# Performance work log

Hardware: AMD Instinct MI355X
Metric: run time of the kernel (lower is better)

Reference implementation:

```python
import jax, jax.numpy as jnp
from jax import lax
import numpy as np

B, T, L, D, TOPK, KC = 8, 4096, 256, 128, 8, 9  # KC = ctx conv kernel size


def setup_inputs() -> dict:
    key = jax.random.key(0)
    ks = jax.random.split(key, 9)
    s = 0.05
    return {
        "x": jax.random.normal(ks[0], (B, T), jnp.float32),
        "lag_embed": jax.random.normal(ks[1], (L + 1, D), jnp.float32) * s,  # nn.Embedding(L+1, d)
        "val_w": jax.random.normal(ks[2], (D, 1), jnp.float32) * s,          # nn.Linear(1, d) weight
        "val_b": jnp.zeros((D,), jnp.float32),
        "conv_w": jax.random.normal(ks[3], (D, 1, KC), jnp.float32) * s,     # Conv1d(1, d, 9) weight (O,I,K)
        "conv_b": jnp.zeros((D,), jnp.float32),
        "ctx_w": jax.random.normal(ks[4], (D, D), jnp.float32) * s,          # ctx_proj
        "ctx_b": jnp.zeros((D,), jnp.float32),
        "wq": jax.random.normal(ks[5], (D, D), jnp.float32) * s,             # Wq (no bias)
        "wk": jax.random.normal(ks[6], (D, D), jnp.float32) * s,             # Wk (no bias)
        "bias_w": jax.random.normal(ks[7], (1, D), jnp.float32) * s,         # bias_head
        "bias_b": jnp.zeros((1,), jnp.float32),
    }


def _lag_bank(x, Lv):
    # Xlags[b, t, l] = x[b, t-(l+1)], left-padded with zeros (per docstring/intended math)
    Bv, Tv = x.shape
    pads = jnp.pad(x, ((0, 0), (Lv, 0)))
    idx = Lv - 1 + jnp.arange(Tv)[:, None] - jnp.arange(Lv)[None, :]  # (T, L)
    return pads[:, idx]  # (B, T, L)


def reference(x, lag_embed, val_w, val_b, conv_w, conv_b, ctx_w, ctx_b, wq, wk, bias_w, bias_b):
    Xlags = _lag_bank(x, L)  # (B, T, L)

    # Causal context conv: left-pad 8 zeros, Conv1d(1, D, 9, padding=0)
    xp = jnp.pad(x, ((0, 0), (KC - 1, 0)))[:, None, :]  # (B, 1, T+8)
    ctx = lax.conv_general_dilated(xp, conv_w, (1,), 'VALID',
                                   dimension_numbers=('NCH', 'OIH', 'NCH'))
    ctx = ctx + conv_b[None, :, None]           # (B, D, T)
    ctx = jnp.transpose(ctx, (0, 2, 1))         # (B, T, D)
    ctx = ctx @ ctx_w.T + ctx_b                 # ctx_proj

    q = ctx @ wq.T                              # (B, T, D)
    # score = <q, Wk Hlag> = <Wk^T q, Hlag>; Hlag = Xlags*val_w + (val_b + lag_embed[1:L+1])
    # is rank-1 in the value -> never materialize the (B,T,L,D) tensor.
    qk = q @ wk                                 # (B, T, D) = Wk^T q
    base = val_b[None, :] + lag_embed[1:L + 1]  # (L, D)
    logits = Xlags * (qk @ val_w[:, 0])[:, :, None] + qk @ base.T  # (B, T, L)

    # top-k sparsification (ties are measure-zero with continuous inputs)
    kth = lax.top_k(logits, TOPK)[0][..., -1:]
    masked = jnp.where(logits >= kth, logits, -jnp.inf)
    w = jax.nn.softmax(masked, axis=-1)         # (B, T, L)

    mu = jnp.sum(w * Xlags, axis=-1) + (ctx @ bias_w.T)[..., 0] + bias_b[0]  # (B, T)
    return mu, w
```

## Files before the change

kernel.cpp:

```cpp
#include <hip/hip_runtime.h>
#include <math.h>

#define D   128
#define LQ  256
#define KCQ 9
#define BQ  8
#define TQ  4096
#define RISK_DELTA 2e-5f
#define WCAP 16384

__global__ void pk1(const float* __restrict__ wk, const float* __restrict__ wq,
                    const float* __restrict__ ctx_w, const float* __restrict__ bias_w,
                    const float* __restrict__ conv_w, const float* __restrict__ val_b,
                    const float* __restrict__ lag_embed,
                    double* __restrict__ T2, double* __restrict__ u, int* __restrict__ wcnt,
                    float* __restrict__ ctx_wT, float* __restrict__ wqT,
                    float* __restrict__ conv_wT, float* __restrict__ baseT) {
    int tid = threadIdx.x;
    int bid = blockIdx.x;
    if (bid < D) {
        int d = bid;
        if (tid < D) {
            double acc = 0.0;
            for (int j = 0; j < D; ++j)
                acc += (double)wk[j * D + d] * (double)wq[j * D + tid];
            T2[d * D + tid] = acc;
            ctx_wT[d * D + tid] = ctx_w[tid * D + d];
            wqT[d * D + tid]    = wq[tid * D + d];
            if (d < KCQ) conv_wT[d * D + tid] = conv_w[tid * KCQ + d];
        }
        baseT[d * LQ + tid] = __fadd_rn(val_b[d], lag_embed[(size_t)(tid + 1) * D + d]);
    } else if (bid == D) {
        if (tid < D) {
            double acc = 0.0;
            for (int dd = 0; dd < D; ++dd)
                acc += (double)bias_w[dd] * (double)ctx_w[dd * D + tid];
            u[tid] = acc;
        }
    } else {
        if (tid == 0) *wcnt = 0;
    }
}

__global__ void pk2(const double* __restrict__ T2, const float* __restrict__ ctx_w,
                    const float* __restrict__ conv_w, const float* __restrict__ conv_b,
                    const float* __restrict__ ctx_b,
                    double* __restrict__ g, double* __restrict__ c1) {
    __shared__ double row[D];
    int d = blockIdx.x, e = threadIdx.x;
    double acc = 0.0;
    for (int j = 0; j < D; ++j)
        acc += T2[d * D + j] * (double)ctx_w[j * D + e];
    row[e] = acc;
    __syncthreads();
    if (e < KCQ) {
        double a = 0.0;
        for (int q = 0; q < D; ++q) a += row[q] * (double)conv_w[q * KCQ + e];
        g[e * D + d] = a;
    } else if (e == KCQ) {
        double a = 0.0;
        for (int q = 0; q < D; ++q) a += row[q] * (double)conv_b[q];
        for (int q = 0; q < D; ++q) a += T2[d * D + q] * (double)ctx_b[q];
        c1[d] = a;
    }
}

__global__ void pk3(const float* __restrict__ lag_embed, const float* __restrict__ val_b,
                    const float* __restrict__ val_w, const float* __restrict__ conv_w,
                    const float* __restrict__ conv_b, const float* __restrict__ ctx_b,
                    const float* __restrict__ bias_w, const float* __restrict__ bias_b,
                    const double* __restrict__ g, const double* __restrict__ c1,
                    const double* __restrict__ u,
                    double* __restrict__ gbT, double* __restrict__ cbv, double* __restrict__ cst) {
    int tid = threadIdx.x;
    if (blockIdx.x < LQ) {
        __shared__ double bl[D];
        int l = blockIdx.x;
        bl[tid] = (double)val_b[tid] + (double)lag_embed[(l + 1) * D + tid];
        __syncthreads();
        if (tid < KCQ) {
            double a = 0.0;
            for (int q = 0; q < D; ++q) a += bl[q] * g[tid * D + q];
            gbT[tid * LQ + l] = a;
        } else if (tid == KCQ) {
            double a = 0.0;
            for (int q = 0; q < D; ++q) a += bl[q] * c1[q];
            cbv[l] = a;
        }
    } else {
        if (tid < KCQ) {
            double a = 0.0, a2 = 0.0;
            for (int q = 0; q < D; ++q) a  += g[tid * D + q] * (double)val_w[q];
            for (int q = 0; q < D; ++q) a2 += u[q] * (double)conv_w[q * KCQ + tid];
            cst[tid]      = a;
            cst[10 + tid] = a2;
        } else if (tid == KCQ) {
            double a = 0.0, a2 = 0.0;
            for (int q = 0; q < D; ++q) a  += c1[q] * (double)val_w[q];
            for (int q = 0; q < D; ++q) a2 += u[q] * (double)conv_b[q];
            for (int q = 0; q < D; ++q) a2 += (double)bias_w[q] * (double)ctx_b[q];
            cst[9]  = a;
            cst[19] = a2 + (double)bias_b[0];
        }
    }
}

__global__ __launch_bounds__(256, 4) void lag_main(
    const float* __restrict__ x, const double* __restrict__ gbT,
    const double* __restrict__ cbv, const double* __restrict__ cst,
    float* __restrict__ muOut, float* __restrict__ wOut,
    int* __restrict__ wcnt, int* __restrict__ wlist) {
    __shared__ float sgb[KCQ * LQ];
    __shared__ float scb[LQ];
    __shared__ float sc[20];
    int tid = threadIdx.x;
    #pragma unroll
    for (int i = 0; i < KCQ; ++i) sgb[i * LQ + tid] = (float)gbT[i * LQ + tid];
    scb[tid] = (float)cbv[tid];
    if (tid < 20) sc[tid] = (float)cst[tid];
    __syncthreads();

    int wave = tid >> 6, lane = tid & 63;
    int row = blockIdx.x * 4 + wave;
    int b = row >> 12;
    int t = row & (TQ - 1);
    const float* xb = x + b * TQ;

    float xw[KCQ];
    #pragma unroll
    for (int k = 0; k < KCQ; ++k) {
        int idx = t - 8 + k;
        xw[k] = (idx >= 0) ? xb[idx] : 0.f;
    }
    float s = sc[9], bias = sc[19];
    #pragma unroll
    for (int k = 0; k < KCQ; ++k) {
        s    = fmaf(sc[k],      xw[k], s);
        bias = fmaf(sc[10 + k], xw[k], bias);
    }

    int l0 = lane * 4;
    float xlag[4];
    #pragma unroll
    for (int i = 0; i < 4; ++i) {
        int idx = t - 1 - (l0 + i);
        xlag[i] = (idx >= 0) ? xb[idx] : 0.f;
    }

    float4 cb4 = *reinterpret_cast<const float4*>(&scb[l0]);
    float lg[4] = {cb4.x, cb4.y, cb4.z, cb4.w};
    #pragma unroll
    for (int k = 0; k < KCQ; ++k) {
        float4 g4 = *reinterpret_cast<const float4*>(&sgb[k * LQ + l0]);
        lg[0] = fmaf(g4.x, xw[k], lg[0]);
        lg[1] = fmaf(g4.y, xw[k], lg[1]);
        lg[2] = fmaf(g4.z, xw[k], lg[2]);
        lg[3] = fmaf(g4.w, xw[k], lg[3]);
    }
    #pragma unroll
    for (int i = 0; i < 4; ++i) lg[i] = fmaf(xlag[i], s, lg[i]);

    const float NEG_INF = -__builtin_inff();
    float wl0 = lg[0], wl1 = lg[1], wl2 = lg[2], wl3 = lg[3];
    float mx = 0.f, thr = 0.f, v9 = 0.f;
    #pragma unroll
    for (int it = 0; it < 9; ++it) {
        float lm = fmaxf(fmaxf(wl0, wl1), fmaxf(wl2, wl3));
        float m = lm;
        #pragma unroll
        for (int off = 32; off >= 1; off >>= 1)
            m = fmaxf(m, __shfl_xor(m, off, 64));
        if (it == 0) mx = m;
        if (it == 7) thr = m;
        if (it == 8) v9 = m;
        if (it < 8) {
            unsigned long long ball = __ballot(lm == m);
            int leader = __ffsll(ball) - 1;
            if (lane == leader) {
                if (wl0 == m)      wl0 = NEG_INF;
                else if (wl1 == m) wl1 = NEG_INF;
                else if (wl2 == m) wl2 = NEG_INF;
                else               wl3 = NEG_INF;
            }
        }
    }

    if ((thr - v9) < RISK_DELTA) {
        if (lane == 0) {
            int pos = atomicAdd(wcnt, 1);
            if (pos < WCAP) wlist[pos] = row;
        }
        return;
    }

    float p[4], psum = 0.f, pmu = 0.f;
    #pragma unroll
    for (int j = 0; j < 4; ++j) {
        p[j] = (lg[j] >= thr) ? __expf(lg[j] - mx) : 0.f;
        psum += p[j];
        pmu = fmaf(p[j], xlag[j], pmu);
    }
    #pragma unroll
    for (int off = 32; off >= 1; off >>= 1) {
        psum += __shfl_xor(psum, off, 64);
        pmu  += __shfl_xor(pmu,  off, 64);
    }
    float inv = 1.f / psum;
    float4 wo = make_float4(p[0] * inv, p[1] * inv, p[2] * inv, p[3] * inv);
    *reinterpret_cast<float4*>(&wOut[(size_t)row * LQ + l0]) = wo;
    if (lane == 0) muOut[row] = fmaf(pmu, inv, bias);
}

__global__ __launch_bounds__(256) void fixer(
    const float* __restrict__ x, const float* __restrict__ wk,
    const float* __restrict__ val_w, const float* __restrict__ conv_b,
    const float* __restrict__ ctx_b, const float* __restrict__ bias_w,
    const float* __restrict__ bias_b,
    const float* __restrict__ ctx_wT, const float* __restrict__ wqT,
    const float* __restrict__ conv_wT, const float* __restrict__ baseT,
    const int* __restrict__ wcnt, const int* __restrict__ wlist,
    float* __restrict__ muOut, float* __restrict__ wOut) {
    __shared__ float sxw[8][KCQ];
    __shared__ float sctxc[8][D];
    __shared__ float sctxp[8][D];
    __shared__ float sq[8][D];
    __shared__ float sqk[8][D];
    __shared__ float ssv[8];
    __shared__ float sbd[8];
    __shared__ float slog[8][LQ];
    __shared__ int   srow[8];

    int cnt = *wcnt;
    if (cnt > WCAP) cnt = WCAP;
    int ngroups = (cnt + 7) >> 3;
    int tid = threadIdx.x;

    for (int gi = blockIdx.x; gi < ngroups; gi += gridDim.x) {
        if (tid < 8) {
            int idx = gi * 8 + tid;
            if (idx >= cnt) idx = cnt - 1;
            srow[tid] = wlist[idx];
        }
        __syncthreads();
        if (tid < 8 * KCQ) {
            int g = tid / KCQ, k = tid % KCQ;
            int row = srow[g]; int b = row >> 12, t = row & (TQ - 1);
            int ii = t - 8 + k;
            sxw[g][k] = (ii >= 0) ? x[b * TQ + ii] : 0.f;
        }
        __syncthreads();

        {
            int d = tid & (D - 1), gh = tid >> 7;
            float cw[KCQ];
            #pragma unroll
            for (int k = 0; k < KCQ; ++k) cw[k] = conv_wT[k * D + d];
            #pragma unroll 1
            for (int g = gh * 4; g < gh * 4 + 4; ++g) {
                float a = 0.f;
                #pragma unroll
                for (int k = 0; k < KCQ; ++k)
                    a = fmaf(cw[k], sxw[g][k], a);
                sctxc[g][d] = __fadd_rn(a, conv_b[d]);
            }
        }
        __syncthreads();

        {
            int e = tid & (D - 1), gh = tid >> 7, g0 = gh * 4;
            float a0 = 0.f, a1 = 0.f, a2 = 0.f, a3 = 0.f;
            float wv0[16], wv1[16];
            #pragma unroll
            for (int u = 0; u < 16; ++u) wv0[u] = ctx_wT[u * D + e];
            #pragma unroll 1
            for (int d2 = 0; d2 < D; d2 += 32) {
                #pragma unroll
                for (int u = 0; u < 16; ++u) wv1[u] = ctx_wT[(d2 + 16 + u) * D + e];
                #pragma unroll
                for (int u = 0; u < 16; ++u) {
                    a0 = fmaf(wv0[u], sctxc[g0 + 0][d2 + u], a0);
                    a1 = fmaf(wv0[u], sctxc[g0 + 1][d2 + u], a1);
                    a2 = fmaf(wv0[u], sctxc[g0 + 2][d2 + u], a2);
                    a3 = fmaf(wv0[u], sctxc[g0 + 3][d2 + u], a3);
                }
                if (d2 + 32 < D) {
                    #pragma unroll
                    for (int u = 0; u < 16; ++u) wv0[u] = ctx_wT[(d2 + 32 + u) * D + e];
                }
                #pragma unroll
                for (int u = 0; u < 16; ++u) {
                    a0 = fmaf(wv1[u], sctxc[g0 + 0][d2 + 16 + u], a0);
                    a1 = fmaf(wv1[u], sctxc[g0 + 1][d2 + 16 + u], a1);
                    a2 = fmaf(wv1[u], sctxc[g0 + 2][d2 + 16 + u], a2);
                    a3 = fmaf(wv1[u], sctxc[g0 + 3][d2 + 16 + u], a3);
                }
            }
            float cb = ctx_b[e];
            sctxp[g0 + 0][e] = __fadd_rn(a0, cb);
            sctxp[g0 + 1][e] = __fadd_rn(a1, cb);
            sctxp[g0 + 2][e] = __fadd_rn(a2, cb);
            sctxp[g0 + 3][e] = __fadd_rn(a3, cb);
        }
        __syncthreads();

        {
            int a = tid & (D - 1), gh = tid >> 7, g0 = gh * 4;
            float a0 = 0.f, a1 = 0.f, a2 = 0.f, a3 = 0.f;
            float wv0[16], wv1[16];
            #pragma unroll
            for (int u = 0; u < 16; ++u) wv0[u] = wqT[u * D + a];
            #pragma unroll 1
            for (int e2 = 0; e2 < D; e2 += 32) {
                #pragma unroll
                for (int u = 0; u < 16; ++u) wv1[u] = wqT[(e2 + 16 + u) * D + a];
                #pragma unroll
                for (int u = 0; u < 16; ++u) {
                    a0 = fmaf(wv0[u], sctxp[g0 + 0][e2 + u], a0);
                    a1 = fmaf(wv0[u], sctxp[g0 + 1][e2 + u], a1);
                    a2 = fmaf(wv0[u], sctxp[g0 + 2][e2 + u], a2);
                    a3 = fmaf(wv0[u], sctxp[g0 + 3][e2 + u], a3);
                }
                if (e2 + 32 < D) {
                    #pragma unroll
                    for (int u = 0; u < 16; ++u) wv0[u] = wqT[(e2 + 32 + u) * D + a];
                }
                #pragma unroll
                for (int u = 0; u < 16; ++u) {
                    a0 = fmaf(wv1[u], sctxp[g0 + 0][e2 + 16 + u], a0);
                    a1 = fmaf(wv1[u], sctxp[g0 + 1][e2 + 16 + u], a1);
                    a2 = fmaf(wv1[u], sctxp[g0 + 2][e2 + 16 + u], a2);
                    a3 = fmaf(wv1[u], sctxp[g0 + 3][e2 + 16 + u], a3);
                }
            }
            sq[g0 + 0][a] = a0;
            sq[g0 + 1][a] = a1;
            sq[g0 + 2][a] = a2;
            sq[g0 + 3][a] = a3;
        }
        __syncthreads();

        {
            int d = tid & (D - 1), gh = tid >> 7, g0 = gh * 4;
            float a0 = 0.f, a1 = 0.f, a2 = 0.f, a3 = 0.f;
            float wv0[16], wv1[16];
            #pragma unroll
            for (int u = 0; u < 16; ++u) wv0[u] = wk[u * D + d];
            #pragma unroll 1
            for (int a2i = 0; a2i < D; a2i += 32) {
                #pragma unroll
                for (int u = 0; u < 16; ++u) wv1[u] = wk[(a2i + 16 + u) * D + d];
                #pragma unroll
                for (int u = 0; u < 16; ++u) {
                    a0 = fmaf(wv0[u], sq[g0 + 0][a2i + u], a0);
                    a1 = fmaf(wv0[u], sq[g0 + 1][a2i + u], a1);
                    a2 = fmaf(wv0[u], sq[g0 + 2][a2i + u], a2);
                    a3 = fmaf(wv0[u], sq[g0 + 3][a2i + u], a3);
                }
                if (a2i + 32 < D) {
                    #pragma unroll
                    for (int u = 0; u < 16; ++u) wv0[u] = wk[(a2i + 32 + u) * D + d];
                }
                #pragma unroll
                for (int u = 0; u < 16; ++u) {
                    a0 = fmaf(wv1[u], sq[g0 + 0][a2i + 16 + u], a0);
                    a1 = fmaf(wv1[u], sq[g0 + 1][a2i + 16 + u], a1);
                    a2 = fmaf(wv1[u], sq[g0 + 2][a2i + 16 + u], a2);
                    a3 = fmaf(wv1[u], sq[g0 + 3][a2i + 16 + u], a3);
                }
            }
            sqk[g0 + 0][d] = a0;
            sqk[g0 + 1][d] = a1;
            sqk[g0 + 2][d] = a2;
            sqk[g0 + 3][d] = a3;
        }
        __syncthreads();

        if (tid < 8) {
            int g = tid;
            float a = 0.f;
            #pragma unroll 1
            for (int d2 = 0; d2 < D; d2 += 16) {
                float vv[16];
                #pragma unroll
                for (int u = 0; u < 16; ++u) vv[u] = val_w[d2 + u];
                #pragma unroll
                for (int u = 0; u < 16; ++u) a = fmaf(sqk[g][d2 + u], vv[u], a);
            }
            ssv[g] = a;
        } else if (tid < 16) {
            int g = tid - 8;
            float a = 0.f;
            #pragma unroll 1
            for (int e2 = 0; e2 < D; e2 += 16) {
                float vv[16];
                #pragma unroll
                for (int u = 0; u < 16; ++u) vv[u] = bias_w[e2 + u];
                #pragma unroll
                for (int u = 0; u < 16; ++u) a = fmaf(sctxp[g][e2 + u], vv[u], a);
            }
            sbd[g] = a;
        }
        __syncthreads();

        {
            int l = tid;
            float c0 = 0.f, c1a = 0.f, c2 = 0.f, c3 = 0.f, c4 = 0.f, c5 = 0.f, c6 = 0.f, c7 = 0.f;
            float bd0[16], bd1[16];
            #pragma unroll
            for (int u = 0; u < 16; ++u) bd0[u] = baseT[u * LQ + l];
            #pragma unroll 1
            for (int d2 = 0; d2 < D; d2 += 32) {
                #pragma unroll
                for (int u = 0; u < 16; ++u) bd1[u] = baseT[(d2 + 16 + u) * LQ + l];
                #pragma unroll
                for (int u = 0; u < 16; ++u) {
                    c0 = fmaf(bd0[u], sqk[0][d2 + u], c0);
                    c1a = fmaf(bd0[u], sqk[1][d2 + u], c1a);
                    c2 = fmaf(bd0[u], sqk[2][d2 + u], c2);
                    c3 = fmaf(bd0[u], sqk[3][d2 + u], c3);
                    c4 = fmaf(bd0[u], sqk[4][d2 + u], c4);
                    c5 = fmaf(bd0[u], sqk[5][d2 + u], c5);
                    c6 = fmaf(bd0[u], sqk[6][d2 + u], c6);
                    c7 = fmaf(bd0[u], sqk[7][d2 + u], c7);
                }
                if (d2 + 32 < D) {
                    #pragma unroll
                    for (int u = 0; u < 16; ++u) bd0[u] = baseT[(d2 + 32 + u) * LQ + l];
                }
                #pragma unroll
                for (int u = 0; u < 16; ++u) {
                    c0 = fmaf(bd1[u], sqk[0][d2 + 16 + u], c0);
                    c1a = fmaf(bd1[u], sqk[1][d2 + 16 + u], c1a);
                    c2 = fmaf(bd1[u], sqk[2][d2 + 16 + u], c2);
                    c3 = fmaf(bd1[u], sqk[3][d2 + 16 + u], c3);
                    c4 = fmaf(bd1[u], sqk[4][d2 + 16 + u], c4);
                    c5 = fmaf(bd1[u], sqk[5][d2 + 16 + u], c5);
                    c6 = fmaf(bd1[u], sqk[6][d2 + 16 + u], c6);
                    c7 = fmaf(bd1[u], sqk[7][d2 + 16 + u], c7);
                }
            }
            float accs[8] = {c0, c1a, c2, c3, c4, c5, c6, c7};
            #pragma unroll
            for (int g = 0; g < 8; ++g) {
                int row = srow[g]; int b = row >> 12, t = row & (TQ - 1);
                int ii = t - 1 - l;
                float xl = (ii >= 0) ? x[b * TQ + ii] : 0.f;
                slog[g][l] = __fadd_rn(__fmul_rn(xl, ssv[g]), accs[g]);
            }
        }
        __syncthreads();

        {
            int wave = tid >> 6, lane = tid & 63;
            #pragma unroll 1
            for (int gg = wave * 2; gg < wave * 2 + 2; ++gg) {
                float lv0 = slog[gg][lane], lv1 = slog[gg][lane + 64];
                float lv2 = slog[gg][lane + 128], lv3 = slog[gg][lane + 192];
                const float NEG_INF = -__builtin_inff();
                float w0 = lv0, w1 = lv1, w2 = lv2, w3 = lv3;
                float mx = 0.f, thr = 0.f;
                #pragma unroll
                for (int it = 0; it < 8; ++it) {
                    float lm = fmaxf(fmaxf(w0, w1), fmaxf(w2, w3));
                    float m = lm;
                    #pragma unroll
                    for (int off = 32; off >= 1; off >>= 1)
                        m = fmaxf(m, __shfl_xor(m, off, 64));
                    if (it == 0) mx = m;
                    thr = m;
                    if (it < 7) {
                        unsigned long long ball = __ballot(lm == m);
                        int leader = __ffsll(ball) - 1;
                        if (lane == leader) {
                            if (w0 == m)      w0 = NEG_INF;
                            else if (w1 == m) w1 = NEG_INF;
                            else if (w2 == m) w2 = NEG_INF;
                            else              w3 = NEG_INF;
                        }
                    }
                }
                int row = srow[gg]; int b = row >> 12, t = row & (TQ - 1);
                float p[4], xlg[4];
                double ps = 0.0;
                float lvs[4] = {lv0, lv1, lv2, lv3};
                #pragma unroll
                for (int j = 0; j < 4; ++j) {
                    int l = lane + 64 * j;
                    int ii = t - 1 - l;
                    xlg[j] = (ii >= 0) ? x[b * TQ + ii] : 0.f;
                    p[j] = (lvs[j] >= thr) ? (float)exp((double)__fsub_rn(lvs[j], mx)) : 0.f;
                    ps += (double)p[j];
                }
                #pragma unroll
                for (int off = 32; off >= 1; off >>= 1)
                    ps += __shfl_xor(ps, off, 64);
                float psf = (float)ps;
                double mud = 0.0;
                #pragma unroll
                for (int j = 0; j < 4; ++j) {
                    float wv = __fdiv_rn(p[j], psf);
                    wOut[(size_t)row * LQ + lane + 64 * j] = wv;
                    mud += (double)__fmul_rn(wv, xlg[j]);
                }
                #pragma unroll
                for (int off = 32; off >= 1; off >>= 1)
                    mud += __shfl_xor(mud, off, 64);
                if (lane == 0) {
                    float m1 = (float)mud;
                    m1 = __fadd_rn(m1, sbd[gg]);
                    m1 = __fadd_rn(m1, bias_b[0]);
                    muOut[row] = m1;
                }
            }
        }
        __syncthreads();
    }
}

extern "C" void kernel_launch(void* const* d_in, const int* in_sizes, int n_in,
                              void* d_out, int out_size, void* d_ws, size_t ws_size,
                              hipStream_t stream) {
    const float* x         = (const float*)d_in[0];
    const float* lag_embed = (const float*)d_in[1];
    const float* val_w     = (const float*)d_in[2];
    const float* val_b     = (const float*)d_in[3];
    const float* conv_w    = (const float*)d_in[4];
    const float* conv_b    = (const float*)d_in[5];
    const float* ctx_w     = (const float*)d_in[6];
    const float* ctx_b     = (const float*)d_in[7];
    const float* wq        = (const float*)d_in[8];
    const float* wk        = (const float*)d_in[9];
    const float* bias_w    = (const float*)d_in[10];
    const float* bias_b    = (const float*)d_in[11];

    char* wsb = (char*)d_ws;
    double* T2  = (double*)wsb;
    double* g   = T2 + 16384;
    double* u   = g + 1152;
    double* c1  = u + 128;
    double* gbT = c1 + 128;
    double* cbv = gbT + 2304;
    double* cst = cbv + 256;
    int* wcnt  = (int*)(wsb + 163840);
    int* wlist = wcnt + 1;
    float* ctx_wT  = (float*)(wsb + 229504);
    float* wqT     = ctx_wT + 16384;
    float* conv_wT = wqT + 16384;
    float* baseT   = conv_wT + 1152;

    float* muOut = (float*)d_out;
    float* wOut  = muOut + BQ * TQ;

    hipLaunchKernelGGL(pk1, dim3(D + 2), dim3(256), 0, stream,
                       wk, wq, ctx_w, bias_w, conv_w, val_b, lag_embed,
                       T2, u, wcnt, ctx_wT, wqT, conv_wT, baseT);
    hipLaunchKernelGGL(pk2, dim3(D), dim3(D), 0, stream, T2, ctx_w, conv_w, conv_b, ctx_b, g, c1);
    hipLaunchKernelGGL(pk3, dim3(LQ + 1), dim3(D), 0, stream,
                       lag_embed, val_b, val_w, conv_w, conv_b, ctx_b, bias_w, bias_b,
                       g, c1, u, gbT, cbv, cst);
    hipLaunchKernelGGL(lag_main, dim3(BQ * TQ / 4), dim3(256), 0, stream,
                       x, gbT, cbv, cst, muOut, wOut, wcnt, wlist);
    hipLaunchKernelGGL(fixer, dim3(256), dim3(256), 0, stream,
                       x, wk, val_w, conv_b, ctx_b, bias_w, bias_b,
                       ctx_wT, wqT, conv_wT, baseT, wcnt, wlist, muOut, wOut);
}
```

Baseline: 101.0 us.

## Process multiple rows per block in lag_main to amortize shared-memory setup

Each lag_main block now loops over 16 row-groups instead of one, so the shared-memory load of the gb/cb/constant tables (converted from double) is amortized across 64 rows, and the grid shrinks by 16x. The top-k removal step drops the ballot/leader selection in favour of branchless per-element comparisons, the overflow path now writes the row normally when the deferral list is full, and the launch-bounds occupancy hint is raised to 8. The risks are reduced parallelism from the smaller grid and slightly different tie handling in the top-k loop.

```diff
diff --git a/kernel.cpp b/kernel.cpp
--- a/kernel.cpp
+++ b/kernel.cpp
@@ -8,6 +8,7 @@
 #define TQ  4096
 #define RISK_DELTA 2e-5f
 #define WCAP 16384
+#define QPB 16
 
 __global__ void pk1(const float* __restrict__ wk, const float* __restrict__ wq,
                     const float* __restrict__ ctx_w, const float* __restrict__ bias_w,
@@ -105,7 +106,7 @@
     }
 }
 
-__global__ __launch_bounds__(256, 4) void lag_main(
+__global__ __launch_bounds__(256, 8) void lag_main(
     const float* __restrict__ x, const double* __restrict__ gbT,
     const double* __restrict__ cbv, const double* __restrict__ cst,
     float* __restrict__ muOut, float* __restrict__ wOut,
@@ -121,94 +122,98 @@
     __syncthreads();
 
     int wave = tid >> 6, lane = tid & 63;
-    int row = blockIdx.x * 4 + wave;
-    int b = row >> 12;
-    int t = row & (TQ - 1);
-    const float* xb = x + b * TQ;
-
-    float xw[KCQ];
-    #pragma unroll
-    for (int k = 0; k < KCQ; ++k) {
-        int idx = t - 8 + k;
-        xw[k] = (idx >= 0) ? xb[idx] : 0.f;
+    int l0 = lane * 4;
+    const float4 cb4 = *reinterpret_cast<const float4*>(&scb[l0]);
+    const float NEG_INF = -__builtin_inff();
+
+    #pragma unroll 1
+    for (int it0 = 0; it0 < QPB; ++it0) {
+        int row = (blockIdx.x * QPB + it0) * 4 + wave;
+        int b = row >> 12;
+        int t = row & (TQ - 1);
+        const float* xb = x + b * TQ;
+
+        float xw[KCQ];
+        #pragma unroll
+        for (int k = 0; k < KCQ; ++k) {
+            int idx = t - 8 + k;
+            xw[k] = (idx >= 0) ? xb[idx] : 0.f;
+        }
+        float s = sc[9], bias = sc[19];
+        #pragma unroll
+        for (int k = 0; k < KCQ; ++k) {
+            s    = fmaf(sc[k],      xw[k], s);
+            bias = fmaf(sc[10 + k], xw[k], bias);
+        }
+
+        float xlag[4];
+        #pragma unroll
+        for (int i = 0; i < 4; ++i) {
+            int idx = t - 1 - (l0 + i);
+            xlag[i] = (idx >= 0) ? xb[idx] : 0.f;
+        }
+
+        float lg[4] = {cb4.x, cb4.y, cb4.z, cb4.w};
+        #pragma unroll
+        for (int k = 0; k < KCQ; ++k) {
+            float4 g4 = *reinterpret_cast<const float4*>(&sgb[k * LQ + l0]);
+            lg[0] = fmaf(g4.x, xw[k], lg[0]);
+            lg[1] = fmaf(g4.y, xw[k], lg[1]);
+            lg[2] = fmaf(g4.z, xw[k], lg[2]);
+            lg[3] = fmaf(g4.w, xw[k], lg[3]);
+        }
+        #pragma unroll
+        for (int i = 0; i < 4; ++i) lg[i] = fmaf(xlag[i], s, lg[i]);
+
+        float wl0 = lg[0], wl1 = lg[1], wl2 = lg[2], wl3 = lg[3];
+        float mx = 0.f, thr = 0.f, v9 = 0.f;
+        #pragma unroll
+        for (int it = 0; it < 9; ++it) {
+            float lm = fmaxf(fmaxf(wl0, wl1), fmaxf(wl2, wl3));
+            float m = lm;
+            #pragma unroll
+            for (int off = 32; off >= 1; off >>= 1)
+                m = fmaxf(m, __shfl_xor(m, off, 64));
+            if (it == 0) mx = m;
+            if (it == 7) thr = m;
+            if (it == 8) v9 = m;
+            if (it < 8) {
+                wl0 = (wl0 == m) ? NEG_INF : wl0;
+                wl1 = (wl1 == m) ? NEG_INF : wl1;
+                wl2 = (wl2 == m) ? NEG_INF : wl2;
+                wl3 = (wl3 == m) ? NEG_INF : wl3;
+            }
+        }
+
+        bool defer = false;
+        if ((thr - v9) < RISK_DELTA) {
+            int pos = 0;
+            if (lane == 0) pos = atomicAdd(wcnt, 1);
+            pos = __shfl(pos, 0, 64);
+            if (pos < WCAP) {
+                if (lane == 0) wlist[pos] = row;
+                defer = true;
+            }
+        }
+        if (!defer) {
+            float p[4], psum = 0.f, pmu = 0.f;
+            #pragma unroll
+            for (int j = 0; j < 4; ++j) {
+                p[j] = (lg[j] >= thr) ? __expf(lg[j] - mx) : 0.f;
+                psum += p[j];
+                pmu = fmaf(p[j], xlag[j], pmu);
+            }
+            #pragma unroll
+            for (int off = 32; off >= 1; off >>= 1) {
+                psum += __shfl_xor(psum, off, 64);
+                pmu  += __shfl_xor(pmu,  off, 64);
+            }
+            float inv = 1.f / psum;
+            float4 wo = make_float4(p[0] * inv, p[1] * inv, p[2] * inv, p[3] * inv);
+            *reinterpret_cast<float4*>(&wOut[(size_t)row * LQ + l0]) = wo;
+            if (lane == 0) muOut[row] = fmaf(pmu, inv, bias);
+        }
     }
-    float s = sc[9], bias = sc[19];
-    #pragma unroll
-    for (int k = 0; k < KCQ; ++k) {
-        s    = fmaf(sc[k],      xw[k], s);
-        bias = fmaf(sc[10 + k], xw[k], bias);
-    }
-
-    int l0 = lane * 4;
-    float xlag[4];
-    #pragma unroll
-    for (int i = 0; i < 4; ++i) {
-        int idx = t - 1 - (l0 + i);
-        xlag[i] = (idx >= 0) ? xb[idx] : 0.f;
-    }
-
-    float4 cb4 = *reinterpret_cast<const float4*>(&scb[l0]);
-    float lg[4] = {cb4.x, cb4.y, cb4.z, cb4.w};
-    #pragma unroll
-    for (int k = 0; k < KCQ; ++k) {
-        float4 g4 = *reinterpret_cast<const float4*>(&sgb[k * LQ + l0]);
-        lg[0] = fmaf(g4.x, xw[k], lg[0]);
-        lg[1] = fmaf(g4.y, xw[k], lg[1]);
-        lg[2] = fmaf(g4.z, xw[k], lg[2]);
-        lg[3] = fmaf(g4.w, xw[k], lg[3]);
-    }
-    #pragma unroll
-    for (int i = 0; i < 4; ++i) lg[i] = fmaf(xlag[i], s, lg[i]);
-
-    const float NEG_INF = -__builtin_inff();
-    float wl0 = lg[0], wl1 = lg[1], wl2 = lg[2], wl3 = lg[3];
-    float mx = 0.f, thr = 0.f, v9 = 0.f;
-    #pragma unroll
-    for (int it = 0; it < 9; ++it) {
-        float lm = fmaxf(fmaxf(wl0, wl1), fmaxf(wl2, wl3));
-        float m = lm;
-        #pragma unroll
-        for (int off = 32; off >= 1; off >>= 1)
-            m = fmaxf(m, __shfl_xor(m, off, 64));
-        if (it == 0) mx = m;
-        if (it == 7) thr = m;
-        if (it == 8) v9 = m;
-        if (it < 8) {
-            unsigned long long ball = __ballot(lm == m);
-            int leader = __ffsll(ball) - 1;
-            if (lane == leader) {
-                if (wl0 == m)      wl0 = NEG_INF;
-                else if (wl1 == m) wl1 = NEG_INF;
-                else if (wl2 == m) wl2 = NEG_INF;
-                else               wl3 = NEG_INF;
-            }
-        }
-    }
-
-    if ((thr - v9) < RISK_DELTA) {
-        if (lane == 0) {
-            int pos = atomicAdd(wcnt, 1);
-            if (pos < WCAP) wlist[pos] = row;
-        }
-        return;
-    }
-
-    float p[4], psum = 0.f, pmu = 0.f;
-    #pragma unroll
-    for (int j = 0; j < 4; ++j) {
-        p[j] = (lg[j] >= thr) ? __expf(lg[j] - mx) : 0.f;
-        psum += p[j];
-        pmu = fmaf(p[j], xlag[j], pmu);
-    }
-    #pragma unroll
-    for (int off = 32; off >= 1; off >>= 1) {
-        psum += __shfl_xor(psum, off, 64);
-        pmu  += __shfl_xor(pmu,  off, 64);
-    }
-    float inv = 1.f / psum;
-    float4 wo = make_float4(p[0] * inv, p[1] * inv, p[2] * inv, p[3] * inv);
-    *reinterpret_cast<float4*>(&wOut[(size_t)row * LQ + l0]) = wo;
-    if (lane == 0) muOut[row] = fmaf(pmu, inv, bias);
 }
 
 __global__ __launch_bounds__(256) void fixer(
@@ -391,12 +396,8 @@
             int g = tid - 8;
             float a = 0.f;
             #pragma unroll 1
-            for (int e2 = 0; e2 < D; e2 += 16) {
-                float vv[16];
-                #pragma unroll
-                for (int u = 0; u < 16; ++u) vv[u] = bias_w[e2 + u];
-                #pragma unroll
-                for (int u = 0; u < 16; ++u) a = fmaf(sctxp[g][e2 + u], vv[u], a);
+            for (int e2 = 0; e2 < D; ++e2) {
+                a = fmaf(sctxp[g][e2], bias_w[e2], a);
             }
             sbd[g] = a;
         }
@@ -558,7 +559,7 @@
     hipLaunchKernelGGL(pk3, dim3(LQ + 1), dim3(D), 0, stream,
                        lag_embed, val_b, val_w, conv_w, conv_b, ctx_b, bias_w, bias_b,
                        g, c1, u, gbT, cbv, cst);
-    hipLaunchKernelGGL(lag_main, dim3(BQ * TQ / 4), dim3(256), 0, stream,
+    hipLaunchKernelGGL(lag_main, dim3(BQ * TQ / (4 * QPB)), dim3(256), 0, stream,
                        x, gbT, cbv, cst, muOut, wOut, wcnt, wlist);
     hipLaunchKernelGGL(fixer, dim3(256), dim3(256), 0, stream,
                        x, wk, val_w, conv_b, ctx_b, bias_w, bias_b,
```

Result: slower. 180.5 us (+78.7%).
